# Optimization experiments

Hardware: AMD Instinct MI355X
Metric: run time of the kernel (lower is better)

## Reference

```python
import jax, jax.numpy as jnp
import numpy as np

H = 20          # hidden_size (pinned by mu0 = zeros(20) in the original)
H2 = 2 * H      # real/imag concatenated state width
SQRT_H = float(np.sqrt(H))


def times_diag(h, theta_row):
    # complex rotation by exp(i*theta), expressed on concatenated [re, im]
    d = jnp.concatenate([theta_row, -theta_row])          # (40,)
    re = jnp.cos(d)
    im = jnp.sin(d)
    h_im = h * im                                          # broadcasts (N,1) or (N,40) -> (N,40)
    swapped = jnp.concatenate([h_im[:, H:], h_im[:, :H]], axis=-1)
    return h * re + swapped


def do_fft(h):
    # torch.fft(x, 2) on shape (1, H, 2): 2D FFT over dims (1, H) == 1D FFT over H, then /sqrt(H)
    c = h[:, :H] + 1j * h[:, H:]
    f = jnp.fft.fft(c, axis=-1) / SQRT_H
    return jnp.concatenate([f.real, f.imag], axis=-1)


def do_ifft(h):
    # torch.ifft is 1/n-normalized; original divides by sqrt(H) again -> unnorm_ifft/(H*sqrt(H))
    c = h[:, :H] + 1j * h[:, H:]
    f = jnp.fft.ifft(c, axis=-1) / SQRT_H
    return jnp.concatenate([f.real, f.imag], axis=-1)


def times_reflection(h, refl):
    vr, vi = refl[:H], refl[H:]
    vstarv = jnp.sum(refl ** 2)
    xr, xi = h[:, :H], h[:, H:]
    s1 = xr @ vr - xi @ vi                                 # (N,)  (matches original a/c coefficient)
    s2 = xr @ vi + xi @ vr                                 # (N,)  (matches original b/d coefficient)
    scale = 2.0 / vstarv
    new_r = xr - scale * (s1[:, None] * vr + s2[:, None] * vi)
    new_i = xi - scale * (s2[:, None] * vr - s1[:, None] * vi)
    return jnp.concatenate([new_r, new_i], axis=-1)


def recurrence(h, theta, reflection):
    h = times_diag(h, theta[0])
    h = do_fft(h)
    h = times_reflection(h, reflection[0])
    # FAITHFUL to original bug: vec_permutation(hidden, self.hidden_size) -> hidden[:, 20]
    h = h[:, H:H + 1]                                      # (N, 1)
    h = times_diag(h, theta[1])                            # broadcasts back to (N, 40)
    h = do_ifft(h)
    h = times_reflection(h, reflection[1])
    h = times_diag(h, theta[2])
    return h


def setup_inputs() -> dict:
    key = jax.random.key(0)
    ks = jax.random.split(key, 6)
    N, T, D = 1024, 512, 128
    inputs = jax.random.normal(ks[0], (N, T, D), dtype=jnp.float32)
    C_w = jax.random.normal(ks[1], (H2, D), dtype=jnp.float32) * (1.0 / np.sqrt(D))
    B_w = jax.random.normal(ks[2], (1, H2), dtype=jnp.float32) * (1.0 / np.sqrt(H2))
    bin_ = float(np.sqrt(6.0 / (2 + H2)))
    reflection = jax.random.uniform(ks[3], (2, H2), dtype=jnp.float32, minval=-bin_, maxval=bin_)
    theta = jax.random.uniform(ks[4], (3, H), dtype=jnp.float32, minval=-np.pi, maxval=np.pi)
    mu0 = jax.random.normal(ks[5], (H,), dtype=jnp.float32) * 0.01
    return {"inputs": inputs, "C_w": C_w, "B_w": B_w, "reflection": reflection, "theta": theta, "mu0": mu0}


def reference(inputs, C_w, B_w, reflection, theta, mu0):
    N, T, _ = inputs.shape
    # precompute input projections once: CLinear(inputs[n,t,:]) for all n,t
    cinp = jnp.einsum('ntd,hd->tnh', inputs, C_w)          # (T, N, 40)
    h0 = jnp.broadcast_to(jnp.concatenate([mu0, -mu0]), (N, H2))

    def step(h, c_t):
        h = c_t + recurrence(h, theta, reflection)
        return h, None

    hT, _ = jax.lax.scan(step, h0, cinp)
    return hT @ B_w.T                                      # (N, 1)
```

## Files before the change

### kernel.cpp

```cpp
#include <hip/hip_runtime.h>
#include <hip/hip_bf16.h>

#define H   20
#define H2  40
#define T   512
#define D   128
#define NN  1024
#define K   (T*D)

__global__ __launch_bounds__(256) void setup_kernel(
    const float* __restrict__ C_w,
    const float* __restrict__ B_w,
    const float* __restrict__ refl,
    const float* __restrict__ theta,
    const float* __restrict__ mu0,
    float* __restrict__ Wout,
    float* __restrict__ extra)
{
    __shared__ double twr[H], twi[H];
    __shared__ double c0t[H], s0t[H], c1t[H], s1t[H], c2t[H], s2t[H];
    __shared__ double v0r_s[H], v0i_s[H], v1r_s[H], v1i_s[H];
    __shared__ double scale0_s, scale1_s;
    __shared__ double a_s[H2];
    __shared__ double fr_s[H], fi_s[H];
    __shared__ double sr_s, si_s;
    __shared__ double w_s[H2];
    __shared__ double g_s, Bw_s;
    __shared__ double lgabs_s;
    __shared__ int gneg_s, gzero_s;
    __shared__ double alpha_s[D], beta_s[D];
    __shared__ double pw_s[T];
    __shared__ int tmin_s;
    __shared__ double c0_s;

    const double PI = 3.141592653589793238462643383279502884;
    const int tid = threadIdx.x;
    const double invsH = 1.0 / sqrt((double)H);

    if (tid < H) {
        double ang = -2.0 * PI * (double)tid / (double)H;
        twr[tid] = cos(ang); twi[tid] = sin(ang);
        double t0 = theta[tid], t1 = theta[H + tid], t2 = theta[2*H + tid];
        c0t[tid] = cos(t0); s0t[tid] = sin(t0);
        c1t[tid] = cos(t1); s1t[tid] = sin(t1);
        c2t[tid] = cos(t2); s2t[tid] = sin(t2);
        v0r_s[tid] = refl[tid];        v0i_s[tid] = refl[H + tid];
        v1r_s[tid] = refl[H2 + tid];   v1i_s[tid] = refl[H2 + H + tid];
    }
    if (tid == 0) {
        double vv0 = 0.0, vv1 = 0.0;
        for (int j = 0; j < H2; j++) {
            double r0 = refl[j], r1 = refl[H2 + j];
            vv0 += r0 * r0; vv1 += r1 * r1;
        }
        scale0_s = 2.0 / vv0; scale1_s = 2.0 / vv1;
    }
    __syncthreads();

    if (tid < H2) {
        int j = tid, p = j % H;
        double vr, vi;
        if (j < H) { vr = c0t[p]; vi = s0t[p]; }
        else       { vr = -s0t[p]; vi = c0t[p]; }
        double sr = 0.0, si = 0.0;
        for (int n = 0; n < H; n++) {
            int m = (n * p) % H;
            double wr = twr[m], wi = twi[m];
            double fr = vr * wr - vi * wi;
            double fi = vr * wi + vi * wr;
            sr += v0r_s[n] * fr - v0i_s[n] * fi;
            si += v0r_s[n] * fi + v0i_s[n] * fr;
        }
        sr *= invsH; si *= invsH;
        double f0i = invsH * vi;
        a_s[j] = f0i - scale0_s * (si * v0r_s[0] - sr * v0i_s[0]);
    }
    if (tid >= 64 && tid < 64 + H) {
        int n = tid - 64;
        double accr = 0.0, acci = 0.0;
        for (int k = 0; k < H; k++) {
            int m = (k * n) % H;
            double wr = twr[m], wi = -twi[m];
            double urk = c1t[k] - s1t[k], uik = c1t[k] + s1t[k];
            accr += urk * wr - uik * wi;
            acci += urk * wi + uik * wr;
        }
        double sc = invsH / (double)H;
        fr_s[n] = accr * sc; fi_s[n] = acci * sc;
    }
    __syncthreads();

    if (tid == 0) {
        double sr = 0.0, si = 0.0;
        for (int n = 0; n < H; n++) {
            sr += v1r_s[n] * fr_s[n] - v1i_s[n] * fi_s[n];
            si += v1r_s[n] * fi_s[n] + v1i_s[n] * fr_s[n];
        }
        sr_s = sr; si_s = si;
    }
    __syncthreads();

    if (tid < H) {
        int n = tid;
        double yr = fr_s[n] - scale1_s * (sr_s * v1r_s[n] + si_s * v1i_s[n]);
        double yi = fi_s[n] - scale1_s * (si_s * v1r_s[n] - sr_s * v1i_s[n]);
        w_s[n]     = yr * c2t[n] - yi * s2t[n];
        w_s[H + n] = yi * c2t[n] + yr * s2t[n];
    }
    __syncthreads();

    if (tid == 0) {
        double g = 0.0, Bw = 0.0;
        for (int j = 0; j < H2; j++) g  += a_s[j] * w_s[j];
        for (int j = 0; j < H2; j++) Bw += (double)B_w[j] * w_s[j];
        g_s = g; Bw_s = Bw;
        gzero_s = (g == 0.0);
        gneg_s  = (g < 0.0);
        lgabs_s = (g == 0.0) ? 0.0 : log2(fabs(g));
    }
    __syncthreads();

    for (int t = tid; t < T - 1; t += blockDim.x) {
        int k = (T - 2) - t;
        double val;
        if (k == 0)          val = 1.0;
        else if (gzero_s)    val = 0.0;
        else {
            val = exp2((double)k * lgabs_s);
            if (gneg_s && (k & 1)) val = -val;
        }
        pw_s[t] = val;
    }
    if (tid < D) {
        double al = 0.0, be = 0.0;
        for (int j = 0; j < H2; j++) {
            double cw = C_w[j * D + tid];
            al += a_s[j] * cw;
            be += (double)B_w[j] * cw;
        }
        alpha_s[tid] = al; beta_s[tid] = be;
    }
    __syncthreads();

    if (tid == 0) {
        double amax = 0.0;
        for (int d2 = 0; d2 < D; d2++) amax = fmax(amax, fabs(alpha_s[d2]));
        double absBw = fabs(Bw_s);
        int tmin = T - 1;
        for (int t = 0; t < T - 1; t++) {
            if (absBw * fabs(pw_s[t]) * amax >= 1e-20) { tmin = t; break; }
        }
        tmin_s = tmin;
        double s0 = 0.0;
        for (int j = 0; j < H; j++) s0 += (a_s[j] - a_s[H + j]) * (double)mu0[j];
        c0_s = Bw_s * g_s * pw_s[0] * s0;
    }
    __syncthreads();

    for (int idx = tid; idx < K; idx += blockDim.x) {
        int t = idx >> 7, d2 = idx & (D - 1);
        double val = (t == T - 1) ? beta_s[d2] : Bw_s * pw_s[t] * alpha_s[d2];
        Wout[idx] = (float)val;
    }
    if (tid == 0) {
        extra[0] = (float)c0_s;
        ((int*)extra)[1] = tmin_s;
    }
}

__global__ __launch_bounds__(512) void dot_kernel(
    const float* __restrict__ x,
    const float* __restrict__ Wv,
    const float* __restrict__ extra,
    float* __restrict__ out)
{
    const int n = blockIdx.x;
    const int tmin = ((const int*)extra)[1];
    const int i0 = tmin << 5;
    const float4* xp = (const float4*)(x + (size_t)n * K);
    const float4* wp = (const float4*)Wv;

    float acc = 0.f;
    for (int i = i0 + threadIdx.x; i < (K >> 2); i += blockDim.x) {
        float4 a = xp[i];
        float4 b = wp[i];
        acc += a.x * b.x + a.y * b.y + a.z * b.z + a.w * b.w;
    }
    for (int off = 32; off > 0; off >>= 1) acc += __shfl_down(acc, off, 64);

    __shared__ float wsum[8];
    const int lane = threadIdx.x & 63, wid = threadIdx.x >> 6;
    if (lane == 0) wsum[wid] = acc;
    __syncthreads();
    if (threadIdx.x == 0) {
        float tot = extra[0];
        const int nw = blockDim.x >> 6;
        for (int wv = 0; wv < nw; wv++) tot += wsum[wv];
        out[n] = tot;
    }
}

extern "C" void kernel_launch(void* const* d_in, const int* in_sizes, int n_in,
                              void* d_out, int out_size, void* d_ws, size_t ws_size,
                              hipStream_t stream) {
    const float* inputs = (const float*)d_in[0];
    const float* C_w    = (const float*)d_in[1];
    const float* B_w    = (const float*)d_in[2];
    const float* refl   = (const float*)d_in[3];
    const float* theta  = (const float*)d_in[4];
    const float* mu0    = (const float*)d_in[5];
    float* out = (float*)d_out;

    float* Wv    = (float*)d_ws;
    float* extra = Wv + K;

    setup_kernel<<<1, 256, 0, stream>>>(C_w, B_w, refl, theta, mu0, Wv, extra);
    dot_kernel<<<NN, 512, 0, stream>>>(inputs, Wv, extra, out);
}
```

Baseline: 355.7 us.

## Factor weight matrix into per-timestep coefficients and per-dim vectors

```diff
diff --git a/kernel.cpp b/kernel.cpp
--- a/kernel.cpp
+++ b/kernel.cpp
@@ -8,14 +8,19 @@
 #define NN  1024
 #define K   (T*D)
 
+#define WS_COEF  0
+#define WS_ALPHA T
+#define WS_BETA  (T + D)
+#define WS_C0    (T + 2*D)
+#define WS_TMIN  (T + 2*D + 1)
+
 __global__ __launch_bounds__(256) void setup_kernel(
     const float* __restrict__ C_w,
     const float* __restrict__ B_w,
     const float* __restrict__ refl,
     const float* __restrict__ theta,
     const float* __restrict__ mu0,
-    float* __restrict__ Wout,
-    float* __restrict__ extra)
+    float* __restrict__ ws)
 {
     __shared__ double twr[H], twi[H];
     __shared__ double c0t[H], s0t[H], c1t[H], s1t[H], c2t[H], s2t[H];
@@ -28,10 +33,9 @@
     __shared__ double g_s, Bw_s;
     __shared__ double lgabs_s;
     __shared__ int gneg_s, gzero_s;
-    __shared__ double alpha_s[D], beta_s[D];
+    __shared__ double alpha_s[D];
     __shared__ double pw_s[T];
-    __shared__ int tmin_s;
-    __shared__ double c0_s;
+    __shared__ double amax_s;
 
     const double PI = 3.141592653589793238462643383279502884;
     const int tid = threadIdx.x;
@@ -130,7 +134,10 @@
             if (gneg_s && (k & 1)) val = -val;
         }
         pw_s[t] = val;
-    }
+        ws[WS_COEF + t] = (float)(Bw_s * val);
+    }
+    if (tid == 0) ws[WS_COEF + T - 1] = 1.0f;
+
     if (tid < D) {
         double al = 0.0, be = 0.0;
         for (int j = 0; j < H2; j++) {
@@ -138,64 +145,65 @@
             al += a_s[j] * cw;
             be += (double)B_w[j] * cw;
         }
-        alpha_s[tid] = al; beta_s[tid] = be;
+        alpha_s[tid] = al;
+        ws[WS_ALPHA + tid] = (float)al;
+        ws[WS_BETA  + tid] = (float)be;
     }
     __syncthreads();
 
     if (tid == 0) {
         double amax = 0.0;
         for (int d2 = 0; d2 < D; d2++) amax = fmax(amax, fabs(alpha_s[d2]));
+        amax_s = amax;
         double absBw = fabs(Bw_s);
         int tmin = T - 1;
         for (int t = 0; t < T - 1; t++) {
             if (absBw * fabs(pw_s[t]) * amax >= 1e-20) { tmin = t; break; }
         }
-        tmin_s = tmin;
         double s0 = 0.0;
         for (int j = 0; j < H; j++) s0 += (a_s[j] - a_s[H + j]) * (double)mu0[j];
-        c0_s = Bw_s * g_s * pw_s[0] * s0;
-    }
-    __syncthreads();
-
-    for (int idx = tid; idx < K; idx += blockDim.x) {
-        int t = idx >> 7, d2 = idx & (D - 1);
-        double val = (t == T - 1) ? beta_s[d2] : Bw_s * pw_s[t] * alpha_s[d2];
-        Wout[idx] = (float)val;
-    }
-    if (tid == 0) {
-        extra[0] = (float)c0_s;
-        ((int*)extra)[1] = tmin_s;
+        ws[WS_C0] = (float)(Bw_s * g_s * pw_s[0] * s0);
+        ((int*)ws)[WS_TMIN] = tmin;
     }
 }
 
-__global__ __launch_bounds__(512) void dot_kernel(
+__global__ __launch_bounds__(256) void dot_kernel(
     const float* __restrict__ x,
-    const float* __restrict__ Wv,
-    const float* __restrict__ extra,
+    const float* __restrict__ ws,
     float* __restrict__ out)
 {
+    __shared__ float coef_s[T];
+    __shared__ float4 a4_s[D/4], b4_s[D/4];
+    __shared__ float wsum[4];
+
+    const int tid = threadIdx.x;
+    coef_s[tid]       = ws[WS_COEF + tid];
+    coef_s[256 + tid] = ws[WS_COEF + 256 + tid];
+    if (tid < D/4)            a4_s[tid]        = ((const float4*)(ws + WS_ALPHA))[tid];
+    else if (tid < D/2)       b4_s[tid - D/4]  = ((const float4*)(ws + WS_BETA))[tid - D/4];
+    const int tmin = ((const int*)ws)[WS_TMIN];
+    __syncthreads();
+
     const int n = blockIdx.x;
-    const int tmin = ((const int*)extra)[1];
     const int i0 = tmin << 5;
     const float4* xp = (const float4*)(x + (size_t)n * K);
-    const float4* wp = (const float4*)Wv;
 
     float acc = 0.f;
-    for (int i = i0 + threadIdx.x; i < (K >> 2); i += blockDim.x) {
-        float4 a = xp[i];
-        float4 b = wp[i];
-        acc += a.x * b.x + a.y * b.y + a.z * b.z + a.w * b.w;
+    for (int i = i0 + tid; i < (K >> 2); i += 256) {
+        int t = i >> 5, q = i & 31;
+        float4 x4 = xp[i];
+        float4 w4 = (t == T - 1) ? b4_s[q] : a4_s[q];
+        float  c  = coef_s[t];
+        acc += c * (x4.x * w4.x + x4.y * w4.y + x4.z * w4.z + x4.w * w4.w);
     }
     for (int off = 32; off > 0; off >>= 1) acc += __shfl_down(acc, off, 64);
 
-    __shared__ float wsum[8];
-    const int lane = threadIdx.x & 63, wid = threadIdx.x >> 6;
+    const int lane = tid & 63, wid = tid >> 6;
     if (lane == 0) wsum[wid] = acc;
     __syncthreads();
-    if (threadIdx.x == 0) {
-        float tot = extra[0];
-        const int nw = blockDim.x >> 6;
-        for (int wv = 0; wv < nw; wv++) tot += wsum[wv];
+    if (tid == 0) {
+        float tot = ws[WS_C0];
+        for (int wv = 0; wv < 4; wv++) tot += wsum[wv];
         out[n] = tot;
     }
 }
@@ -210,10 +218,8 @@
     const float* theta  = (const float*)d_in[4];
     const float* mu0    = (const float*)d_in[5];
     float* out = (float*)d_out;
-
-    float* Wv    = (float*)d_ws;
-    float* extra = Wv + K;
-
-    setup_kernel<<<1, 256, 0, stream>>>(C_w, B_w, refl, theta, mu0, Wv, extra);
-    dot_kernel<<<NN, 512, 0, stream>>>(inputs, Wv, extra, out);
+    float* ws  = (float*)d_ws;
+
+    setup_kernel<<<1, 256, 0, stream>>>(C_w, B_w, refl, theta, mu0, ws);
+    dot_kernel<<<NN, 256, 0, stream>>>(inputs, ws, out);
 }
```

Measured after the change: 339.1 us. 1.05x faster.
